# Kernel tuning notes

Measured on AMD Instinct MI355X. Metric: run time of the kernel, lower is better.

## Reference

```python
import jax, jax.numpy as jnp
import numpy as np

F_SIZE = 1000   # feature_size
FIELDS = 39     # field_size
K = 40          # ffm embedding dim
BATCH = 4096
LAYERS = [1024, 512, 256]


def setup_inputs() -> dict:
    key = jax.random.key(0)
    ks = jax.random.split(key, 12)
    inp = {
        "X": jax.random.normal(ks[0], (BATCH, F_SIZE), dtype=jnp.float32),
        "w1": jax.random.normal(ks[1], (F_SIZE,), dtype=jnp.float32) * 0.01,
        "b": jnp.full((1,), 0.5, dtype=jnp.float32),
        "nfk": jax.random.normal(ks[2], (F_SIZE, FIELDS, K), dtype=jnp.float32) * 0.01,
        "f2f": jax.random.randint(ks[3], (F_SIZE,), 0, FIELDS, dtype=jnp.int32),
    }
    dims = [F_SIZE] + LAYERS
    for i in range(len(LAYERS)):
        fan_in, fan_out = dims[i], dims[i + 1]
        scale = np.sqrt(6.0 / (fan_in + fan_out)).astype(np.float32)
        inp[f"deepW{i}"] = jax.random.uniform(ks[4 + i], (fan_in, fan_out), dtype=jnp.float32, minval=-scale, maxval=scale)
        inp[f"deepB{i}"] = jnp.zeros((fan_out,), dtype=jnp.float32)
    scale = np.sqrt(6.0 / (LAYERS[-1] + 1)).astype(np.float32)
    inp["outW"] = jax.random.uniform(ks[10], (LAYERS[-1], 1), dtype=jnp.float32, minval=-scale, maxval=scale)
    inp["outB"] = jnp.zeros((1,), dtype=jnp.float32)
    return inp


def reference(X, w1, b, nfk, f2f, deepW0, deepB0, deepW1, deepB1, deepW2, deepB2, outW, outB):
    # --- linear term: sum_i w1[i]*X[:,i] + b ---
    linear = X @ w1 + b[0]                                  # [B]

    # --- field-aware interaction ---
    # A[i, j, :] = nfk[i, f2f[j], :]  (gather over fields)
    F = nfk.shape[0]
    A = nfk[jnp.arange(F)[:, None], f2f[None, :], :]        # [F, F, K]
    # S[i, j] = <nfk[i, f2f[j]], nfk[j, f2f[i]]> -- batch-independent scalar
    S = jnp.einsum('ijk,jik->ij', A, A)                     # [F, F]
    M = jnp.triu(S, 1)                                      # keep i < j pairs only
    # sum_{i<j} S[i,j] * X[:,i] * X[:,j]
    interaction = jnp.sum((X @ M) * X, axis=1)              # [B]

    # --- deep part (train=False: no dropout) ---
    h = jax.nn.relu(X @ deepW0 + deepB0)
    h = jax.nn.relu(h @ deepW1 + deepB1)
    h = jax.nn.relu(h @ deepW2 + deepB2)
    deep = (h @ outW + outB).reshape(-1)                    # [B]

    out_sum = linear + interaction + deep                   # logits [B]
    return out_sum
```

## Files before the change

### kernel.cpp

```cpp
#include <hip/hip_runtime.h>


#define BATCH   4096
#define FSZ     1000
#define NFIELDS 39
#define KDIM    40

typedef __attribute__((ext_vector_type(8))) short short8v;
typedef __attribute__((ext_vector_type(4))) float f32x4;

__device__ __forceinline__ short f2bf(float f) {
  unsigned u = __builtin_bit_cast(unsigned, f);
  u += 0x7fff + ((u >> 16) & 1);
  return (short)(u >> 16);
}
__device__ __forceinline__ float bf2f(unsigned short h) {
  unsigned u = (unsigned)h << 16;
  return __builtin_bit_cast(float, u);
}

typedef const __attribute__((address_space(1))) unsigned int* gas_ptr;
typedef __attribute__((address_space(3))) unsigned int* las_ptr;
__device__ __forceinline__ void gload16(const void* g, void* l) {
  __builtin_amdgcn_global_load_lds((gas_ptr)g, (las_ptr)l, 16, 0, 0);
}

__device__ __forceinline__ void transp32(
    const float* __restrict__ in, short* __restrict__ out, int idx, int nx,
    int K_in, int N_in, int Kpad, float (*t)[33], int tid)
{
  int n0 = (idx % nx) * 32, k0 = (idx / nx) * 32;
  int tx = tid & 31, ty = tid >> 5;
  #pragma unroll
  for (int i = 0; i < 32; i += 8) {
    int k = k0 + ty + i, n = n0 + tx;
    t[ty + i][tx] = (k < K_in && n < N_in) ? in[(size_t)k * N_in + n] : 0.f;
  }
  __syncthreads();
  #pragma unroll
  for (int i = 0; i < 32; i += 8) {
    int n = n0 + ty + i, k = k0 + tx;
    if (n < N_in && k < Kpad) out[(size_t)n * Kpad + k] = f2bf(t[tx][ty + i]);
  }
}

__global__ __launch_bounds__(256) void prep_a_kernel(
    const float* __restrict__ X, const float* __restrict__ nfk,
    const float* __restrict__ W0, const float* __restrict__ W1,
    const float* __restrict__ W2,
    short* __restrict__ Xb, short* __restrict__ B12,
    short* __restrict__ Wt1, short* __restrict__ Wt2,
    float* __restrict__ nfkT)
{
  __shared__ float tbuf[32][33];
  const int bid = blockIdx.x, tid = threadIdx.x;
  if (bid < 4096) {
    int k = tid * 4;
    short4 o = make_short4(0, 0, 0, 0);
    if (k < FSZ) {
      float4 v = *(const float4*)(X + (size_t)bid * FSZ + k);
      o = make_short4(f2bf(v.x), f2bf(v.y), f2bf(v.z), f2bf(v.w));
    }
    *(short4*)(Xb + (size_t)bid * 1024 + k) = o;
  } else if (bid < 5120) {
    transp32(W0, B12 + 1024 * 1024, bid - 4096, 32, 1000, 1024, 1024, tbuf, tid);
  } else if (bid < 5632) {
    transp32(W1, Wt1, bid - 5120, 16, 1024, 512, 1024, tbuf, tid);
  } else if (bid < 5760) {
    transp32(W2, Wt2, bid - 5632, 8, 512, 256, 512, tbuf, tid);
  } else {
    int idx = bid - 5760;
    int g = idx >> 2, jc = idx & 3;
    int j = jc * 256 + tid;
    if (j < FSZ && g < NFIELDS) {
      const float4* src = (const float4*)(nfk + ((size_t)j * NFIELDS + g) * KDIM);
      float4* dst = (float4*)(nfkT + ((size_t)g * FSZ + j) * KDIM);
      #pragma unroll
      for (int t = 0; t < KDIM / 4; ++t) dst[t] = src[t];
    }
  }
}

__global__ __launch_bounds__(256) void prep_b_kernel(
    const float* __restrict__ nfk, const float* __restrict__ nfkT,
    const int* __restrict__ f2f, short* __restrict__ B12)
{
  __shared__ float C[NFIELDS * 44];
  const int n = blockIdx.x, tid = threadIdx.x;
  if (n < FSZ) {
    for (int t = tid; t < NFIELDS * KDIM; t += 256)
      C[(t / KDIM) * 44 + (t % KDIM)] = nfk[(size_t)n * (NFIELDS * KDIM) + t];
  }
  __syncthreads();
  int fn = (n < FSZ) ? f2f[n] : 0;
  const float* pbase = nfkT + (size_t)fn * FSZ * KDIM;
  #pragma unroll
  for (int kk = 0; kk < 4; ++kk) {
    int k = kk * 256 + tid;
    float s = 0.f;
    if (n < FSZ && k < n) {
      int fk = f2f[k];
      const float4* p = (const float4*)(pbase + (size_t)k * KDIM);
      const float4* q = (const float4*)&C[fk * 44];
      #pragma unroll
      for (int t = 0; t < KDIM / 4; ++t) {
        float4 a = p[t], b = q[t];
        s += a.x * b.x + a.y * b.y + a.z * b.z + a.w * b.w;
      }
    }
    B12[(size_t)n * 1024 + k] = f2bf(s);
  }
}

template<int BM, int BN, int EPI>
__global__ __launch_bounds__(256) void gemm_mfma(
    const short* __restrict__ A, const short* __restrict__ Bt,
    const float* __restrict__ bias, void* __restrict__ Cout,
    int N, int K,
    const short* __restrict__ Xb, const float* __restrict__ w1,
    float* __restrict__ partial,
    const float* __restrict__ c1, const float* __restrict__ c2)
{
  constexpr int AM = BM / 32, AN = BN / 32;
  __shared__ __align__(16) short As[2][BM * 64];
  __shared__ __align__(16) short Bs[2][BN * 64];
  __shared__ float pbuf[2][BM];

  const int nwgx = gridDim.x;
  const int lin  = blockIdx.y * nwgx + blockIdx.x;
  const int cpx  = (nwgx * gridDim.y) >> 3;
  const int slin = (lin & 7) * cpx + (lin >> 3);
  const int bx   = slin % nwgx;
  const int by   = slin / nwgx;

  const int tid  = threadIdx.x;
  const int wid  = tid >> 6;
  const int lane = tid & 63;
  const int wr   = wid >> 1, wc = wid & 1;
  const int row0 = by * BM;
  const int col0 = bx * BN;

  const int lr8   = lane >> 3;
  const int cbase = (lane & 7) * 16;

  f32x4 acc[AM][AN];
  #pragma unroll
  for (int m = 0; m < AM; ++m)
    #pragma unroll
    for (int n = 0; n < AN; ++n) acc[m][n] = (f32x4)(0.f);

  auto stage = [&](int p, int k0) {
    #pragma unroll
    for (int j = 0; j < BM / 32; ++j) {
      int i = j * 4 + wid;
      int r = i * 8 + lr8;
      int cb = cbase ^ ((r & 7) << 4);
      gload16((const char*)A + (((size_t)(row0 + r) * K + k0) << 1) + cb,
              (char*)&As[p][0] + i * 1024);
    }
    #pragma unroll
    for (int j = 0; j < BN / 32; ++j) {
      int i = j * 4 + wid;
      int r = i * 8 + lr8;
      int cb = cbase ^ ((r & 7) << 4);
      gload16((const char*)Bt + (((size_t)(col0 + r) * K + k0) << 1) + cb,
              (char*)&Bs[p][0] + i * 1024);
    }
  };

  auto compute = [&](int p) {
    #pragma unroll
    for (int kk = 0; kk < 2; ++kk) {
      const int cb = kk * 64 + (lane >> 4) * 16;
      short8v a[AM], b[AN];
      #pragma unroll
      for (int m = 0; m < AM; ++m) {
        int r = wr * (BM / 2) + m * 16 + (lane & 15);
        a[m] = *(const short8v*)((const char*)&As[p][0] + r * 128 + (cb ^ ((r & 7) << 4)));
      }
      #pragma unroll
      for (int n = 0; n < AN; ++n) {
        int r = wc * (BN / 2) + n * 16 + (lane & 15);
        b[n] = *(const short8v*)((const char*)&Bs[p][0] + r * 128 + (cb ^ ((r & 7) << 4)));
      }
      #pragma unroll
      for (int m = 0; m < AM; ++m)
        #pragma unroll
        for (int n = 0; n < AN; ++n)
          acc[m][n] = __builtin_amdgcn_mfma_f32_16x16x32_bf16(a[m], b[n], acc[m][n], 0, 0, 0);
    }
  };

  int nt = K >> 6;
  if (EPI == 0 && bx < 8) {
    int need = bx * 2 + 2;
    nt = nt < need ? nt : need;
  }

  stage(0, 0);
  __syncthreads();
  for (int t = 0; t < nt; ++t) {
    if (t + 1 < nt) stage((t + 1) & 1, (t + 1) << 6);
    compute(t & 1);
    __syncthreads();
  }

  const int cr = (lane >> 4) * 4;
  const int cc = lane & 15;

  if (EPI == 0) {
    if (bx < 8) {
      float rsum[AM * 4];
      #pragma unroll
      for (int i = 0; i < AM * 4; ++i) rsum[i] = 0.f;
      #pragma unroll
      for (int m = 0; m < AM; ++m) {
        #pragma unroll
        for (int n = 0; n < AN; ++n) {
          int gc = col0 + wc * (BN / 2) + n * 16 + cc;
          float w1v = (gc < FSZ) ? w1[gc] : 0.f;
          #pragma unroll
          for (int r = 0; r < 4; ++r) {
            int gr = row0 + wr * (BM / 2) + m * 16 + cr + r;
            float xv = bf2f((unsigned short)Xb[(size_t)gr * 1024 + gc]);
            rsum[m * 4 + r] = fmaf(acc[m][n][r] + w1v, xv, rsum[m * 4 + r]);
          }
        }
      }
      #pragma unroll
      for (int mask = 1; mask < 16; mask <<= 1)
        #pragma unroll
        for (int i = 0; i < AM * 4; ++i)
          rsum[i] += __shfl_xor(rsum[i], mask, 64);
      if (cc == 0) {
        #pragma unroll
        for (int m = 0; m < AM; ++m)
          #pragma unroll
          for (int r = 0; r < 4; ++r)
            pbuf[wc][wr * (BM / 2) + m * 16 + cr + r] = rsum[m * 4 + r];
      }
      __syncthreads();
      if (tid < BM)
        partial[(size_t)(row0 + tid) * 8 + bx] = pbuf[0][tid] + pbuf[1][tid];
    } else {
      #pragma unroll
      for (int m = 0; m < AM; ++m) {
        #pragma unroll
        for (int n = 0; n < AN; ++n) {
          int gc = col0 - 1024 + wc * (BN / 2) + n * 16 + cc;
          float bv = bias[gc];
          #pragma unroll
          for (int r = 0; r < 4; ++r) {
            int gr = row0 + wr * (BM / 2) + m * 16 + cr + r;
            float v = fmaxf(acc[m][n][r] + bv, 0.f);
            ((short*)Cout)[(size_t)gr * 1024 + gc] = f2bf(v);
          }
        }
      }
    }
  } else if (EPI == 1) {
    #pragma unroll
    for (int m = 0; m < AM; ++m) {
      #pragma unroll
      for (int n = 0; n < AN; ++n) {
        int gc = col0 + wc * (BN / 2) + n * 16 + cc;
        float bv = bias[gc];
        #pragma unroll
        for (int r = 0; r < 4; ++r) {
          int gr = row0 + wr * (BM / 2) + m * 16 + cr + r;
          float v = fmaxf(acc[m][n][r] + bv, 0.f);
          ((short*)Cout)[(size_t)gr * N + gc] = f2bf(v);
        }
      }
    }
  } else {
    float rsum[AM * 4];
    #pragma unroll
    for (int i = 0; i < AM * 4; ++i) rsum[i] = 0.f;
    #pragma unroll
    for (int m = 0; m < AM; ++m) {
      #pragma unroll
      for (int n = 0; n < AN; ++n) {
        int gc = col0 + wc * (BN / 2) + n * 16 + cc;
        float bv = bias[gc];
        float ow = w1[gc];
        #pragma unroll
        for (int r = 0; r < 4; ++r) {
          float v = fmaxf(acc[m][n][r] + bv, 0.f);
          rsum[m * 4 + r] = fmaf(v, ow, rsum[m * 4 + r]);
        }
      }
    }
    #pragma unroll
    for (int mask = 1; mask < 16; mask <<= 1)
      #pragma unroll
      for (int i = 0; i < AM * 4; ++i)
        rsum[i] += __shfl_xor(rsum[i], mask, 64);
    if (cc == 0) {
      #pragma unroll
      for (int m = 0; m < AM; ++m)
        #pragma unroll
        for (int r = 0; r < 4; ++r)
          pbuf[wc][wr * (BM / 2) + m * 16 + cr + r] = rsum[m * 4 + r];
    }
    __syncthreads();
    if (tid < BM) {
      int gr = row0 + tid;
      const float4* pp = (const float4*)(partial + (size_t)gr * 8);
      float4 u = pp[0], v = pp[1];
      ((float*)Cout)[gr] = pbuf[0][tid] + pbuf[1][tid]
          + u.x + u.y + u.z + u.w + v.x + v.y + v.z + v.w + c1[0] + c2[0];
    }
  }
}

extern "C" void kernel_launch(void* const* d_in, const int* in_sizes, int n_in,
                              void* d_out, int out_size, void* d_ws, size_t ws_size,
                              hipStream_t stream) {
  const float* X   = (const float*)d_in[0];
  const float* w1  = (const float*)d_in[1];
  const float* bsc = (const float*)d_in[2];
  const float* nfk = (const float*)d_in[3];
  const int*   f2f = (const int*)d_in[4];
  const float* W0  = (const float*)d_in[5];
  const float* B0  = (const float*)d_in[6];
  const float* W1  = (const float*)d_in[7];
  const float* B1  = (const float*)d_in[8];
  const float* W2  = (const float*)d_in[9];
  const float* B2  = (const float*)d_in[10];
  const float* oW  = (const float*)d_in[11];
  const float* oB  = (const float*)d_in[12];
  float* out = (float*)d_out;

  char* ws = (char*)d_ws;
  short* Xb   = (short*)(ws);
  short* B12  = (short*)(ws + 8388608);
  short* Wt1  = (short*)(ws + 12582912);
  short* Wt2  = (short*)(ws + 13631488);
  float* part = (float*)(ws + 13893632);
  short* h0   = (short*)(ws + 14680064);
  short* h1   = (short*)(ws + 23068672);
  float* nfkT = (float*)(ws + 27262976);

  prep_a_kernel<<<5916, 256, 0, stream>>>(X, nfk, W0, W1, W2,
                                          Xb, B12, Wt1, Wt2, nfkT);
  prep_b_kernel<<<1024, 256, 0, stream>>>(nfk, nfkT, f2f, B12);
  gemm_mfma<128, 128, 0><<<dim3(16, 32), 256, 0, stream>>>(
      Xb, B12, B0, h0, 2048, 1024, Xb, w1, part, nullptr, nullptr);
  gemm_mfma<64, 64, 1><<<dim3(8, 64), 256, 0, stream>>>(
      h0, Wt1, B1, h1, 512, 1024, nullptr, nullptr, nullptr, nullptr, nullptr);
  gemm_mfma<32, 256, 3><<<dim3(1, 128), 256, 0, stream>>>(
      h1, Wt2, B2, out, 256, 512, nullptr, oW, part, bsc, oB);
}
```

Measured before the change: 73.90 us.

## Store nfkT in bf16, balance prep_b rows, enlarge first GEMM tile

The transposed nfk copy is now stored as bf16, which halves the bytes prep_b reads per dot product. prep_b now runs half as many blocks, and each block handles a short row n and its long mirror row 1023-n, so the triangular work is spread evenly. The GEMM template gains explicit per-wave tile sizes, and the first GEMM moves to a 256x128 tile with 8 waves (512 threads). The bf16 interaction coefficients lose some precision, and the larger tile leaves fewer blocks to fill the GPU.

```diff
diff --git a/kernel.cpp b/kernel.cpp
--- a/kernel.cpp
+++ b/kernel.cpp
@@ -50,7 +50,7 @@
     const float* __restrict__ W2,
     short* __restrict__ Xb, short* __restrict__ B12,
     short* __restrict__ Wt1, short* __restrict__ Wt2,
-    float* __restrict__ nfkT)
+    unsigned short* __restrict__ nfkT)
 {
   __shared__ float tbuf[32][33];
   const int bid = blockIdx.x, tid = threadIdx.x;
@@ -74,46 +74,56 @@
     int j = jc * 256 + tid;
     if (j < FSZ && g < NFIELDS) {
       const float4* src = (const float4*)(nfk + ((size_t)j * NFIELDS + g) * KDIM);
-      float4* dst = (float4*)(nfkT + ((size_t)g * FSZ + j) * KDIM);
-      #pragma unroll
-      for (int t = 0; t < KDIM / 4; ++t) dst[t] = src[t];
+      short4* dst = (short4*)(nfkT + ((size_t)g * FSZ + j) * KDIM);
+      #pragma unroll
+      for (int t = 0; t < KDIM / 4; ++t) {
+        float4 v = src[t];
+        dst[t] = make_short4(f2bf(v.x), f2bf(v.y), f2bf(v.z), f2bf(v.w));
+      }
     }
   }
 }
 
 __global__ __launch_bounds__(256) void prep_b_kernel(
-    const float* __restrict__ nfk, const float* __restrict__ nfkT,
+    const float* __restrict__ nfk, const unsigned short* __restrict__ nfkT,
     const int* __restrict__ f2f, short* __restrict__ B12)
 {
   __shared__ float C[NFIELDS * 44];
-  const int n = blockIdx.x, tid = threadIdx.x;
-  if (n < FSZ) {
-    for (int t = tid; t < NFIELDS * KDIM; t += 256)
-      C[(t / KDIM) * 44 + (t % KDIM)] = nfk[(size_t)n * (NFIELDS * KDIM) + t];
-  }
-  __syncthreads();
-  int fn = (n < FSZ) ? f2f[n] : 0;
-  const float* pbase = nfkT + (size_t)fn * FSZ * KDIM;
+  const int tid = threadIdx.x;
   #pragma unroll
-  for (int kk = 0; kk < 4; ++kk) {
-    int k = kk * 256 + tid;
-    float s = 0.f;
-    if (n < FSZ && k < n) {
-      int fk = f2f[k];
-      const float4* p = (const float4*)(pbase + (size_t)k * KDIM);
-      const float4* q = (const float4*)&C[fk * 44];
-      #pragma unroll
-      for (int t = 0; t < KDIM / 4; ++t) {
-        float4 a = p[t], b = q[t];
-        s += a.x * b.x + a.y * b.y + a.z * b.z + a.w * b.w;
-      }
-    }
-    B12[(size_t)n * 1024 + k] = f2bf(s);
-  }
-}
-
-template<int BM, int BN, int EPI>
-__global__ __launch_bounds__(256) void gemm_mfma(
+  for (int ri = 0; ri < 2; ++ri) {
+    const int n = ri ? (1023 - (int)blockIdx.x) : (int)blockIdx.x;
+    __syncthreads();
+    if (n < FSZ) {
+      for (int t = tid; t < NFIELDS * KDIM; t += 256)
+        C[(t / KDIM) * 44 + (t % KDIM)] = nfk[(size_t)n * (NFIELDS * KDIM) + t];
+    }
+    __syncthreads();
+    int fn = (n < FSZ) ? f2f[n] : 0;
+    const unsigned short* pbase = nfkT + (size_t)fn * FSZ * KDIM;
+    #pragma unroll
+    for (int kk = 0; kk < 4; ++kk) {
+      int k = kk * 256 + tid;
+      float s = 0.f;
+      if (n < FSZ && k < n) {
+        int fk = f2f[k];
+        const short8v* p = (const short8v*)(pbase + (size_t)k * KDIM);
+        const float* q = &C[fk * 44];
+        #pragma unroll
+        for (int t = 0; t < 5; ++t) {
+          short8v v = p[t];
+          #pragma unroll
+          for (int e = 0; e < 8; ++e)
+            s = fmaf(bf2f((unsigned short)v[e]), q[t * 8 + e], s);
+        }
+      }
+      B12[(size_t)n * 1024 + k] = f2bf(s);
+    }
+  }
+}
+
+template<int BM, int BN, int WM, int WN, int EPI>
+__global__ __launch_bounds__((BM / WM) * (BN / WN) * 64) void gemm_mfma(
     const short* __restrict__ A, const short* __restrict__ Bt,
     const float* __restrict__ bias, void* __restrict__ Cout,
     int N, int K,
@@ -121,7 +131,13 @@
     float* __restrict__ partial,
     const float* __restrict__ c1, const float* __restrict__ c2)
 {
-  constexpr int AM = BM / 32, AN = BN / 32;
+  constexpr int WAVES_M = BM / WM, WAVES_N = BN / WN;
+  constexpr int NW = WAVES_M * WAVES_N;
+  constexpr int AM = WM / 16, AN = WN / 16;
+  constexpr int CA = BM / 8;
+  constexpr int CB = BN / 8;
+  static_assert(CA % NW == 0 && CB % NW == 0, "chunk split");
+  static_assert(WAVES_N == 2, "pbuf sum assumes 2 col-waves");
   __shared__ __align__(16) short As[2][BM * 64];
   __shared__ __align__(16) short Bs[2][BN * 64];
   __shared__ float pbuf[2][BM];
@@ -136,7 +152,7 @@
   const int tid  = threadIdx.x;
   const int wid  = tid >> 6;
   const int lane = tid & 63;
-  const int wr   = wid >> 1, wc = wid & 1;
+  const int wr   = wid / WAVES_N, wc = wid % WAVES_N;
   const int row0 = by * BM;
   const int col0 = bx * BN;
 
@@ -151,16 +167,16 @@
 
   auto stage = [&](int p, int k0) {
     #pragma unroll
-    for (int j = 0; j < BM / 32; ++j) {
-      int i = j * 4 + wid;
+    for (int j = 0; j < CA / NW; ++j) {
+      int i = j * NW + wid;
       int r = i * 8 + lr8;
       int cb = cbase ^ ((r & 7) << 4);
       gload16((const char*)A + (((size_t)(row0 + r) * K + k0) << 1) + cb,
               (char*)&As[p][0] + i * 1024);
     }
     #pragma unroll
-    for (int j = 0; j < BN / 32; ++j) {
-      int i = j * 4 + wid;
+    for (int j = 0; j < CB / NW; ++j) {
+      int i = j * NW + wid;
       int r = i * 8 + lr8;
       int cb = cbase ^ ((r & 7) << 4);
       gload16((const char*)Bt + (((size_t)(col0 + r) * K + k0) << 1) + cb,
@@ -175,12 +191,12 @@
       short8v a[AM], b[AN];
       #pragma unroll
       for (int m = 0; m < AM; ++m) {
-        int r = wr * (BM / 2) + m * 16 + (lane & 15);
+        int r = wr * WM + m * 16 + (lane & 15);
         a[m] = *(const short8v*)((const char*)&As[p][0] + r * 128 + (cb ^ ((r & 7) << 4)));
       }
       #pragma unroll
       for (int n = 0; n < AN; ++n) {
-        int r = wc * (BN / 2) + n * 16 + (lane & 15);
+        int r = wc * WN + n * 16 + (lane & 15);
         b[n] = *(const short8v*)((const char*)&Bs[p][0] + r * 128 + (cb ^ ((r & 7) << 4)));
       }
       #pragma unroll
@@ -217,11 +233,11 @@
       for (int m = 0; m < AM; ++m) {
         #pragma unroll
         for (int n = 0; n < AN; ++n) {
-          int gc = col0 + wc * (BN / 2) + n * 16 + cc;
+          int gc = col0 + wc * WN + n * 16 + cc;
           float w1v = (gc < FSZ) ? w1[gc] : 0.f;
           #pragma unroll
           for (int r = 0; r < 4; ++r) {
-            int gr = row0 + wr * (BM / 2) + m * 16 + cr + r;
+            int gr = row0 + wr * WM + m * 16 + cr + r;
             float xv = bf2f((unsigned short)Xb[(size_t)gr * 1024 + gc]);
             rsum[m * 4 + r] = fmaf(acc[m][n][r] + w1v, xv, rsum[m * 4 + r]);
           }
@@ -237,7 +253,7 @@
         for (int m = 0; m < AM; ++m)
           #pragma unroll
           for (int r = 0; r < 4; ++r)
-            pbuf[wc][wr * (BM / 2) + m * 16 + cr + r] = rsum[m * 4 + r];
+            pbuf[wc][wr * WM + m * 16 + cr + r] = rsum[m * 4 + r];
       }
       __syncthreads();
       if (tid < BM)
@@ -247,11 +263,11 @@
       for (int m = 0; m < AM; ++m) {
         #pragma unroll
         for (int n = 0; n < AN; ++n) {
-          int gc = col0 - 1024 + wc * (BN / 2) + n * 16 + cc;
+          int gc = col0 - 1024 + wc * WN + n * 16 + cc;
           float bv = bias[gc];
           #pragma unroll
           for (int r = 0; r < 4; ++r) {
-            int gr = row0 + wr * (BM / 2) + m * 16 + cr + r;
+            int gr = row0 + wr * WM + m * 16 + cr + r;
             float v = fmaxf(acc[m][n][r] + bv, 0.f);
             ((short*)Cout)[(size_t)gr * 1024 + gc] = f2bf(v);
           }
@@ -263,11 +279,11 @@
     for (int m = 0; m < AM; ++m) {
       #pragma unroll
       for (int n = 0; n < AN; ++n) {
-        int gc = col0 + wc * (BN / 2) + n * 16 + cc;
+        int gc = col0 + wc * WN + n * 16 + cc;
         float bv = bias[gc];
         #pragma unroll
         for (int r = 0; r < 4; ++r) {
-          int gr = row0 + wr * (BM / 2) + m * 16 + cr + r;
+          int gr = row0 + wr * WM + m * 16 + cr + r;
           float v = fmaxf(acc[m][n][r] + bv, 0.f);
           ((short*)Cout)[(size_t)gr * N + gc] = f2bf(v);
         }
@@ -281,7 +297,7 @@
     for (int m = 0; m < AM; ++m) {
       #pragma unroll
       for (int n = 0; n < AN; ++n) {
-        int gc = col0 + wc * (BN / 2) + n * 16 + cc;
+        int gc = col0 + wc * WN + n * 16 + cc;
         float bv = bias[gc];
         float ow = w1[gc];
         #pragma unroll
@@ -301,7 +317,7 @@
       for (int m = 0; m < AM; ++m)
         #pragma unroll
         for (int r = 0; r < 4; ++r)
-          pbuf[wc][wr * (BM / 2) + m * 16 + cr + r] = rsum[m * 4 + r];
+          pbuf[wc][wr * WM + m * 16 + cr + r] = rsum[m * 4 + r];
     }
     __syncthreads();
     if (tid < BM) {
@@ -340,15 +356,15 @@
   float* part = (float*)(ws + 13893632);
   short* h0   = (short*)(ws + 14680064);
   short* h1   = (short*)(ws + 23068672);
-  float* nfkT = (float*)(ws + 27262976);
+  unsigned short* nfkT = (unsigned short*)(ws + 27262976);
 
   prep_a_kernel<<<5916, 256, 0, stream>>>(X, nfk, W0, W1, W2,
                                           Xb, B12, Wt1, Wt2, nfkT);
-  prep_b_kernel<<<1024, 256, 0, stream>>>(nfk, nfkT, f2f, B12);
-  gemm_mfma<128, 128, 0><<<dim3(16, 32), 256, 0, stream>>>(
+  prep_b_kernel<<<512, 256, 0, stream>>>(nfk, nfkT, f2f, B12);
+  gemm_mfma<256, 128, 64, 64, 0><<<dim3(16, 16), 512, 0, stream>>>(
       Xb, B12, B0, h0, 2048, 1024, Xb, w1, part, nullptr, nullptr);
-  gemm_mfma<64, 64, 1><<<dim3(8, 64), 256, 0, stream>>>(
+  gemm_mfma<64, 64, 32, 32, 1><<<dim3(8, 64), 256, 0, stream>>>(
       h0, Wt1, B1, h1, 512, 1024, nullptr, nullptr, nullptr, nullptr, nullptr);
-  gemm_mfma<32, 256, 3><<<dim3(1, 128), 256, 0, stream>>>(
+  gemm_mfma<32, 256, 16, 128, 3><<<dim3(1, 128), 256, 0, stream>>>(
       h1, Wt2, B2, out, 256, 512, nullptr, oW, part, bsc, oB);
 }
```

Result: no change. 75.20 us (+1.8%).
